# Optimization experiments

Hardware: AMD Instinct MI355X
Metric: run time of the kernel (lower is better)

Reference implementation:

```python
import jax, jax.numpy as jnp
import numpy as np

N = 8192
IN_DIM = 512
OUT_DIM = 512
TASK_DIM = 64
NEG_INF = -9.0e15  # matches torch's -9000000000000000.0 mask value


def setup_inputs() -> dict:
    key = jax.random.key(0)
    ks = jax.random.split(key, 12)
    def lin(k, fan_in, fan_out):
        kw, kb = jax.random.split(k)
        bound = 1.0 / np.sqrt(fan_in)
        W = jax.random.uniform(kw, (fan_in, fan_out), minval=-bound, maxval=bound, dtype=jnp.float32)
        b = jax.random.uniform(kb, (fan_out,), minval=-bound, maxval=bound, dtype=jnp.float32)
        return W, b
    h = jax.random.normal(ks[0], (N, IN_DIM), dtype=jnp.float32)
    z = jax.random.normal(ks[1], (N, TASK_DIM), dtype=jnp.float32)
    adj = jax.random.randint(ks[2], (N, N), 0, 2, dtype=jnp.int32)
    Wm, bm = lin(ks[3], IN_DIM, OUT_DIM)
    Wg, bg = lin(ks[4], IN_DIM + TASK_DIM, OUT_DIM)
    Wk, bk = lin(ks[5], IN_DIM, OUT_DIM)
    Wq, bq = lin(ks[6], OUT_DIM, OUT_DIM)
    a = jax.random.normal(ks[7], (OUT_DIM * 2, 1), dtype=jnp.float32)
    return {"h": h, "adj": adj, "z": z, "Wm": Wm, "bm": bm, "Wg": Wg, "bg": bg,
            "Wk": Wk, "bk": bk, "Wq": Wq, "bq": bq, "a": a}


def reference(h, adj, z, Wm, bm, Wg, bg, Wk, bk, Wq, bq, a):
    # raw message + task-conditioned gate
    raw_message = jax.nn.relu(h @ Wm + bm)                       # [N, D]
    gate = jax.nn.sigmoid(jnp.concatenate([h, z], axis=1) @ Wg + bg)  # [N, D]
    gated_message = gate * raw_message                           # [N, D]
    gate_l1_loss = jnp.sum(jnp.abs(gate)) / gate.size
    # attention scores: e[i,j] = leaky_relu(k_j . a[:D] + q_i . a[D:])
    # (decomposes the [N,N,2D] concat @ a without materializing it)
    q = gated_message @ Wq + bq                                  # [N, D]
    k = h @ Wk + bk                                              # [N, D]
    sk = k @ a[:OUT_DIM, 0]                                      # [N] key term (varies over j)
    sq = q @ a[OUT_DIM:, 0]                                      # [N] query term (varies over i)
    e = jax.nn.leaky_relu(sq[:, None] + sk[None, :])             # [N, N]
    attention = jnp.where(adj > 0, e, NEG_INF)
    attention = jax.nn.softmax(attention, axis=1)                # [N, N]
    agg_message = attention.T @ gated_message                    # [N, D]
    h_new = (agg_message + h) / 2
    return h_new, gate_l1_loss
```

## Files before the change

kernel.cpp:

```cpp
#include <hip/hip_runtime.h>

typedef unsigned short u16;
typedef unsigned char u8;
typedef unsigned long long u64;
typedef short s16x8 __attribute__((ext_vector_type(8)));
typedef float f32x4 __attribute__((ext_vector_type(4)));
typedef int i32x4 __attribute__((ext_vector_type(4)));
typedef int i32x8 __attribute__((ext_vector_type(8)));

#define NN 8192
#define DD 512
#define KCAT 576

__device__ __forceinline__ u16 f2bf(float f) {
  unsigned u = __float_as_uint(f);
  unsigned r = u + 0x7fffu + ((u >> 16) & 1u);
  return (u16)(r >> 16);
}
__device__ __forceinline__ float bf2f(u16 s) {
  return __uint_as_float(((unsigned)s) << 16);
}
__device__ __forceinline__ void gld16(const void* g, void* l) {
  __builtin_amdgcn_global_load_lds((const __attribute__((address_space(1))) void*)g,
                                   (__attribute__((address_space(3))) void*)l, 16, 0, 0);
}
__device__ __forceinline__ int pk8(float f0, float f1, float f2, float f3) {
  int p = __builtin_amdgcn_cvt_pk_fp8_f32(f0, f1, 0, 0);
  p = __builtin_amdgcn_cvt_pk_fp8_f32(f2, f3, p, 1);
  return p;
}

__global__ void k_prep(const float* __restrict__ Wk, const float* __restrict__ Wq,
                       const float* __restrict__ bk, const float* __restrict__ bq,
                       const float* __restrict__ a, const float* __restrict__ Wm,
                       const float* __restrict__ Wg, const float* __restrict__ h,
                       const float* __restrict__ z, float* __restrict__ wk_a,
                       float* __restrict__ wq_a, float* __restrict__ sc,
                       u16* __restrict__ WcT, u16* __restrict__ X) {
  const int b = blockIdx.x, t = threadIdx.x;
  if (b < 5) {
    if (b < 2) {
      int c = b * 256 + t;
      float s = 0.f;
      for (int d = 0; d < 512; d++) s += Wk[(size_t)c * 512 + d] * a[d];
      wk_a[c] = s;
    } else if (b < 4) {
      int c = (b - 2) * 256 + t;
      float s = 0.f;
      for (int d = 0; d < 512; d++) s += Wq[(size_t)c * 512 + d] * a[512 + d];
      wq_a[c] = s;
    } else {
      __shared__ float red[8];
      int lane = t & 63, w = t >> 6;
      float s1 = bk[t] * a[t] + bk[t + 256] * a[t + 256];
      float s2 = bq[t] * a[512 + t] + bq[t + 256] * a[768 + t];
      #pragma unroll
      for (int o = 32; o >= 1; o >>= 1) { s1 += __shfl_down(s1, o); s2 += __shfl_down(s2, o); }
      if (lane == 0) { red[w] = s1; red[4 + w] = s2; }
      __syncthreads();
      if (t == 0) {
        sc[0] = red[0] + red[1] + red[2] + red[3];
        sc[1] = red[4] + red[5] + red[6] + red[7];
      }
    }
  } else if (b < 293) {
    int tid = (b - 5) * 256 + t;
    int n = tid / 72, g = tid % 72;
    int lg = (g & ~7) | ((g & 7) ^ (n & 7));
    int k0 = lg * 8;
    s16x8 o;
    #pragma unroll
    for (int e = 0; e < 8; e++) {
      int k = k0 + e;
      float val;
      if (n < 512) val = (k < 512) ? Wm[(size_t)k * 512 + n] : 0.f;
      else         val = Wg[(size_t)k * 512 + (n - 512)];
      o[e] = (short)f2bf(val);
    }
    *(s16x8*)&WcT[(size_t)n * KCAT + g * 8] = o;
  } else {
    int tid = (b - 293) * 256 + t;
    int i = tid / 72, g = tid % 72;
    int lg = (g & ~7) | ((g & 7) ^ (i & 7));
    int k0 = lg * 8;
    s16x8 o;
    if (k0 < 512) {
      const f32x4* s = (const f32x4*)(h + (size_t)i * 512 + k0);
      f32x4 v0 = s[0], v1 = s[1];
      #pragma unroll
      for (int e = 0; e < 4; e++) { o[e] = (short)f2bf(v0[e]); o[e + 4] = (short)f2bf(v1[e]); }
    } else {
      const f32x4* s = (const f32x4*)(z + (size_t)i * 64 + (k0 - 512));
      f32x4 v0 = s[0], v1 = s[1];
      #pragma unroll
      for (int e = 0; e < 4; e++) { o[e] = (short)f2bf(v0[e]); o[e + 4] = (short)f2bf(v1[e]); }
    }
    *(s16x8*)&X[(size_t)i * KCAT + g * 8] = o;
  }
}

__global__ __launch_bounds__(256) void k_gemm1(const u16* __restrict__ X,
    const u16* __restrict__ W, const float* __restrict__ bm, const float* __restrict__ bg,
    u16* __restrict__ rm, u16* __restrict__ gate, float* __restrict__ l1part) {
  __shared__ __align__(16) u16 As[128 * 64];
  __shared__ __align__(16) u16 Bs[128 * 64];
  __shared__ float red[4];
  const int t = threadIdx.x, bid = blockIdx.x;
  const int i0 = (bid & 63) * 128, n0 = (bid >> 6) * 128;
  const int lane = t & 63, w = t >> 6;
  const int lr = lane & 15, lh = lane >> 4;
  const int wm = (w >> 1) * 64, wn = (w & 1) * 64;
  const f32x4 vz = {0.f, 0.f, 0.f, 0.f};
  f32x4 acc[4][4];
  #pragma unroll
  for (int a_ = 0; a_ < 4; a_++)
    #pragma unroll
    for (int b_ = 0; b_ < 4; b_++) acc[a_][b_] = vz;

  for (int step = 0; step < 9; step++) {
    const int kk = step * 64;
    __syncthreads();
    #pragma unroll
    for (int c = 0; c < 4; c++) {
      int L = c * 256 + t;
      int row = L >> 3, ch = L & 7;
      gld16(X + (size_t)(i0 + row) * KCAT + kk + ch * 8, &As[L * 8]);
      gld16(W + (size_t)(n0 + row) * KCAT + kk + ch * 8, &Bs[L * 8]);
    }
    asm volatile("s_waitcnt vmcnt(0)" ::: "memory");
    __syncthreads();
    #pragma unroll
    for (int ks = 0; ks < 2; ks++) {
      s16x8 af[4], bfv[4];
      #pragma unroll
      for (int mr = 0; mr < 4; mr++) {
        int row = wm + mr * 16 + lr;
        int ch = (ks * 4 + lh) ^ (row & 7);
        af[mr] = *(const s16x8*)&As[row * 64 + ch * 8];
      }
      #pragma unroll
      for (int nr = 0; nr < 4; nr++) {
        int nn = wn + nr * 16 + lr;
        int ch = (ks * 4 + lh) ^ (nn & 7);
        bfv[nr] = *(const s16x8*)&Bs[nn * 64 + ch * 8];
      }
      #pragma unroll
      for (int mr = 0; mr < 4; mr++)
        #pragma unroll
        for (int nr = 0; nr < 4; nr++)
          acc[mr][nr] = __builtin_amdgcn_mfma_f32_16x16x32_bf16(af[mr], bfv[nr], acc[mr][nr], 0, 0, 0);
    }
  }
  float lsum = 0.f;
  #pragma unroll
  for (int nr = 0; nr < 4; nr++) {
    int nn = n0 + wn + nr * 16 + lr;
    bool ismsg = nn < 512;
    float bias = ismsg ? bm[nn] : bg[nn - 512];
    #pragma unroll
    for (int mr = 0; mr < 4; mr++) {
      #pragma unroll
      for (int r = 0; r < 4; r++) {
        int row = i0 + wm + mr * 16 + lh * 4 + r;
        float v0 = acc[mr][nr][r] + bias;
        if (ismsg) {
          rm[(size_t)row * 512 + nn] = f2bf(fmaxf(v0, 0.f));
        } else {
          float g = 1.f / (1.f + __expf(-v0));
          gate[(size_t)row * 512 + (nn - 512)] = f2bf(g);
          lsum += g;
        }
      }
    }
  }
  #pragma unroll
  for (int o = 32; o >= 1; o >>= 1) lsum += __shfl_down(lsum, o);
  if (lane == 0) red[w] = lsum;
  __syncthreads();
  if (t == 0) l1part[bid] = red[0] + red[1] + red[2] + red[3];
}

__global__ __launch_bounds__(256) void k_rowact(const u16* __restrict__ rm,
    const u16* __restrict__ gate, const float* __restrict__ h,
    const float* __restrict__ wk_a, const float* __restrict__ wq_a,
    const float* __restrict__ sc, u16* __restrict__ gm, float* __restrict__ skv,
    float* __restrict__ sqv, float* __restrict__ uu, float* __restrict__ vv) {
  __shared__ float red[8];
  const int i = blockIdx.x, t = threadIdx.x;
  const int lane = t & 63, w = t >> 6;
  float sqp = 0.f, skp = 0.f;
  #pragma unroll
  for (int rep = 0; rep < 2; rep++) {
    int d = rep * 256 + t;
    float g = bf2f(gate[(size_t)i * 512 + d]);
    float r = bf2f(rm[(size_t)i * 512 + d]);
    float p = g * r;
    gm[(size_t)i * 512 + d] = f2bf(p);
    sqp += p * wq_a[d];
    skp += h[(size_t)i * 512 + d] * wk_a[d];
  }
  #pragma unroll
  for (int o = 32; o >= 1; o >>= 1) { sqp += __shfl_down(sqp, o); skp += __shfl_down(skp, o); }
  if (lane == 0) { red[w] = skp; red[4 + w] = sqp; }
  __syncthreads();
  if (t == 0) {
    float skt = red[0] + red[1] + red[2] + red[3] + sc[0];
    float sqt = red[4] + red[5] + red[6] + red[7] + sc[1];
    skv[i] = skt; sqv[i] = sqt;
    uu[i] = __expf(skt); vv[i] = __expf(0.01f * skt);
  }
}

__global__ __launch_bounds__(256) void k_pack(const int* __restrict__ adj, u64* __restrict__ bits) {
  __shared__ u16 nib[512];
  const int t = threadIdx.x;
  const size_t i = blockIdx.x;
  #pragma unroll
  for (int k = 0; k < 2; k++) {
    const int4* src = (const int4*)(adj + i * NN + (size_t)(t + 256 * k) * 16);
    unsigned m = 0;
    #pragma unroll
    for (int q = 0; q < 4; q++) {
      int4 v = src[q];
      m |= (v.x > 0 ? 1u : 0u) << (4 * q);
      m |= (v.y > 0 ? 2u : 0u) << (4 * q);
      m |= (v.z > 0 ? 4u : 0u) << (4 * q);
      m |= (v.w > 0 ? 8u : 0u) << (4 * q);
    }
    nib[k * 256 + t] = (u16)m;
  }
  __syncthreads();
  if (t < 128) bits[i * 128 + t] = *(const u64*)&nib[t * 4];
}

__global__ __launch_bounds__(256) void k_stats(const u64* __restrict__ bits,
    const float* __restrict__ sk, const float* __restrict__ uu, const float* __restrict__ vv,
    const float* __restrict__ sq, float* __restrict__ P, float* __restrict__ Q) {
  const int t = threadIdx.x, lane = t & 63, wv = t >> 6;
  const int i = blockIdx.x * 4 + wv;
  const float sqi = sq[i];
  const float nsq = -sqi;
  const u64* brow = bits + (size_t)i * 128;
  float zp = 0.f, zn = 0.f, m_loc = -3.0e38f;
  for (int k = 0; k < 128; k++) {
    u64 word = brow[k];
    float skj = sk[k * 64 + lane];
    float uj = uu[k * 64 + lane];
    float vj = vv[k * 64 + lane];
    m_loc = fmaxf(m_loc, skj);
    bool msk = (word >> lane) & 1ULL;
    bool pos = skj > nsq;
    zp += (msk && pos) ? uj : 0.f;
    zn += (msk && !pos) ? vj : 0.f;
  }
  #pragma unroll
  for (int o = 32; o >= 1; o >>= 1) {
    zp += __shfl_down(zp, o);
    zn += __shfl_down(zn, o);
    m_loc = fmaxf(m_loc, __shfl_down(m_loc, o));
  }
  if (lane == 0) {
    float xk = sqi + m_loc;
    float m_i = xk >= 0.f ? xk : 0.01f * xk;
    float ep = __expf(sqi - m_i), en = __expf(0.01f * sqi - m_i);
    float Z = ep * zp + en * zn;
    float inv = 1.0f / Z;
    P[i] = ep * inv;
    Q[i] = en * inv;
  }
}

__global__ __launch_bounds__(256) void k_tgm8(const u16* __restrict__ gm, u8* __restrict__ gmT8) {
  __shared__ __align__(16) u16 tile[64][72];
  const int bid = blockIdx.x;
  const int ti = bid & 127, td = bid >> 7;
  const int t = threadIdx.x;
  #pragma unroll
  for (int rep = 0; rep < 2; rep++) {
    int L = rep * 256 + t;
    int row = L >> 3, ch = L & 7;
    s16x8 val = *(const s16x8*)(gm + (size_t)(ti * 64 + row) * 512 + td * 64 + ch * 8);
    *(s16x8*)&tile[row][ch * 8] = val;
  }
  __syncthreads();
  const int dl = t >> 2, lc = t & 3;
  const int d = td * 64 + dl;
  const int chg = ti * 4 + lc;
  i32x4 o;
  #pragma unroll
  for (int q = 0; q < 4; q++) {
    int ib = lc * 16 + q * 4;
    o[q] = pk8(bf2f(tile[ib][dl]) * 16.f, bf2f(tile[ib + 1][dl]) * 16.f,
               bf2f(tile[ib + 2][dl]) * 16.f, bf2f(tile[ib + 3][dl]) * 16.f);
  }
  *(i32x4*)(gmT8 + (size_t)d * NN + (chg >> 3) * 128 + ((chg & 7) ^ (d & 7)) * 16) = o;
}

__global__ __launch_bounds__(256) void k_tgm(const u16* __restrict__ gm, u16* __restrict__ gmT) {
  __shared__ __align__(16) u16 tile[64][72];
  const int bid = blockIdx.x;
  const int ti = bid & 127, td = bid >> 7;
  const int t = threadIdx.x;
  #pragma unroll
  for (int rep = 0; rep < 2; rep++) {
    int L = rep * 256 + t;
    int row = L >> 3, ch = L & 7;
    s16x8 val = *(const s16x8*)(gm + (size_t)(ti * 64 + row) * 512 + td * 64 + ch * 8);
    *(s16x8*)&tile[row][ch * 8] = val;
  }
  __syncthreads();
  #pragma unroll
  for (int rep = 0; rep < 2; rep++) {
    int L = rep * 256 + t;
    int dr = L >> 3, ig = L & 7;
    int d = td * 64 + dr;
    s16x8 o;
    #pragma unroll
    for (int e = 0; e < 8; e++) o[e] = (short)tile[ig * 8 + e][dr];
    *(s16x8*)(gmT + (size_t)d * NN + ti * 64 + (ig ^ (d & 7)) * 8) = o;
  }
}

__global__ __launch_bounds__(256) void k_rowstats(const int* __restrict__ adj,
    const float* __restrict__ sk, const float* __restrict__ sq,
    u64* __restrict__ bits, float* __restrict__ P, float* __restrict__ Q) {
  __shared__ float sks[NN];
  __shared__ u64 bw[128];
  __shared__ float red[8];
  const int i = blockIdx.x, t = threadIdx.x;
  const int lane = t & 63, w = t >> 6;
  const int* arow = adj + (size_t)i * NN;
  float kmax = -3.0e38f;
  for (int c = 0; c < 32; c++) {
    int j = c * 256 + t;
    int av = arow[j];
    float skj = sk[j];
    sks[j] = skj;
    bool bit = av > 0;
    u64 m = __ballot(bit);
    if (lane == 0) bw[c * 4 + w] = m;
    if (bit) kmax = fmaxf(kmax, skj);
  }
  #pragma unroll
  for (int o = 32; o >= 1; o >>= 1) kmax = fmaxf(kmax, __shfl_down(kmax, o));
  if (lane == 0) red[w] = kmax;
  __syncthreads();
  float K = fmaxf(fmaxf(red[0], red[1]), fmaxf(red[2], red[3]));
  float sqi = sq[i];
  float xk = sqi + K;
  float m_i = xk >= 0.f ? xk : 0.01f * xk;
  float s = 0.f;
  for (int c = 0; c < 32; c++) {
    int j = c * 256 + t;
    u64 mw = bw[c * 4 + w];
    float xx = sqi + sks[j];
    float f = xx >= 0.f ? xx : 0.01f * xx;
    float e = __expf(f - m_i);
    if ((mw >> lane) & 1ULL) s += e;
  }
  #pragma unroll
  for (int o = 32; o >= 1; o >>= 1) s += __shfl_down(s, o);
  if (lane == 0) red[4 + w] = s;
  __syncthreads();
  if (t == 0) {
    float Z = red[4] + red[5] + red[6] + red[7];
    float inv = 1.0f / Z;
    P[i] = __expf(sqi - m_i) * inv;
    Q[i] = __expf(0.01f * sqi - m_i) * inv;
  }
  if (t < 128) bits[(size_t)i * 128 + t] = bw[t];
}

__global__ void k_bitT(const u64* __restrict__ bits, u64* __restrict__ bitT) {
  int wid = blockIdx.x * 4 + (threadIdx.x >> 6);
  int ti = wid & 127, tj = wid >> 7;
  int lane = threadIdx.x & 63;
  u64 w = bits[(size_t)(ti * 64 + lane) * 128 + tj];
  u64 out = 0;
  #pragma unroll
  for (int jj = 0; jj < 64; jj++) {
    u64 b = __ballot((int)((w >> jj) & 1ULL));
    if (jj == lane) out = b;
  }
  bitT[(size_t)(tj * 64 + lane) * 128 + ti] = out;
}

__global__ __launch_bounds__(256) void k_attgen8(const u64* __restrict__ bitT,
    const float* __restrict__ P, const float* __restrict__ Q, const float* __restrict__ sq,
    const float* __restrict__ u, const float* __restrict__ v, const float* __restrict__ sk,
    u8* __restrict__ attT8) {
  const int t = threadIdx.x, bid = blockIdx.x;
  const int jt = bid >> 1, ih = bid & 1;
  const int j0 = jt * 16;
  const int i0 = ih * 4096 + t * 16;
  f32x4 Pv[4], Qv[4], Sv[4];
  #pragma unroll
  for (int q = 0; q < 4; q++) {
    Pv[q] = *(const f32x4*)(P + i0 + q * 4);
    Qv[q] = *(const f32x4*)(Q + i0 + q * 4);
    Sv[q] = *(const f32x4*)(sq + i0 + q * 4);
  }
  const int widx = i0 >> 6;
  const int bsh = (t & 3) * 16;
  const int chg = i0 >> 4;
  const int wnd = chg >> 3, cs = chg & 7;
  #pragma unroll 2
  for (int r = 0; r < 16; r++) {
    const int j = j0 + r;
    const float uj = u[j] * 256.f, vj = v[j] * 256.f, nskj = -sk[j];
    const u64 w64 = bitT[(size_t)j * 128 + widx];
    const unsigned m16 = (unsigned)(w64 >> bsh) & 0xFFFFu;
    i32x4 o;
    #pragma unroll
    for (int q = 0; q < 4; q++) {
      float f[4];
      #pragma unroll
      for (int e = 0; e < 4; e++) {
        bool pos = Sv[q][e] > nskj;
        float val = pos ? Pv[q][e] * uj : Qv[q][e] * vj;
        f[e] = ((m16 >> (q * 4 + e)) & 1u) ? val : 0.f;
      }
      o[q] = pk8(f[0], f[1], f[2], f[3]);
    }
    *(i32x4*)(attT8 + (size_t)j * NN + wnd * 128 + ((cs ^ (j & 7)) * 16)) = o;
  }
}

__device__ __forceinline__ i32x8 ld_frag8(const u8* base, int row, int lh) {
  const int c0 = ((2 * lh) ^ (row & 7)) * 16;
  const int c1 = ((2 * lh + 1) ^ (row & 7)) * 16;
  i32x4 lo = *(const i32x4*)(base + row * 128 + c0);
  i32x4 hi = *(const i32x4*)(base + row * 128 + c1);
  i32x8 r;
  r[0] = lo[0]; r[1] = lo[1]; r[2] = lo[2]; r[3] = lo[3];
  r[4] = hi[0]; r[5] = hi[1]; r[6] = hi[2]; r[7] = hi[3];
  return r;
}

__global__ __launch_bounds__(256) void k_aggr8(const u8* __restrict__ attT8,
    const u8* __restrict__ gmT8, u16* __restrict__ pb) {
  __shared__ __align__(16) u8 As[128 * 128];
  __shared__ __align__(16) u8 Bs[128 * 128];
  const int t = threadIdx.x, bid = blockIdx.x;
  const int lid = (bid & 7) * 128 + (bid >> 3);
  const int dt = lid & 3, jt = (lid >> 2) & 63, split = lid >> 8;
  const int j0 = jt * 128, d0 = dt * 128;
  const int lane = t & 63, w = t >> 6;
  const int lr = lane & 15, lh = lane >> 4;
  const int wm = (w >> 1) * 64, wn = (w & 1) * 64;
  const f32x4 vz = {0.f, 0.f, 0.f, 0.f};
  f32x4 acc[4][4];
  #pragma unroll
  for (int a_ = 0; a_ < 4; a_++)
    #pragma unroll
    for (int b_ = 0; b_ < 4; b_++) acc[a_][b_] = vz;

  for (int step = 0; step < 16; step++) {
    const int ss = split * 16 + step;
    __syncthreads();
    #pragma unroll
    for (int c = 0; c < 4; c++) {
      int idx = c * 256 + t;
      int row = idx >> 3, ch = idx & 7;
      gld16(attT8 + (size_t)(j0 + row) * NN + (size_t)ss * 128 + ch * 16, &As[idx * 16]);
      gld16(gmT8 + (size_t)(d0 + row) * NN + (size_t)ss * 128 + ch * 16, &Bs[idx * 16]);
    }
    asm volatile("s_waitcnt vmcnt(0)" ::: "memory");
    __syncthreads();
    i32x8 af[4], bfv[4];
    #pragma unroll
    for (int mr = 0; mr < 4; mr++) af[mr] = ld_frag8(As, wm + mr * 16 + lr, lh);
    #pragma unroll
    for (int nr = 0; nr < 4; nr++) bfv[nr] = ld_frag8(Bs, wn + nr * 16 + lr, lh);
    #pragma unroll
    for (int mr = 0; mr < 4; mr++)
      #pragma unroll
      for (int nr = 0; nr < 4; nr++)
        acc[mr][nr] = __builtin_amdgcn_mfma_scale_f32_16x16x128_f8f6f4(
            af[mr], bfv[nr], acc[mr][nr], 0, 0,
            0, 0x77777777,
            0, 0x7B7B7B7B);
  }
  u16* pbs = pb + (size_t)split * NN * 512;
  #pragma unroll
  for (int mr = 0; mr < 4; mr++) {
    #pragma unroll
    for (int nr = 0; nr < 4; nr++) {
      int dn = d0 + wn + nr * 16 + lr;
      #pragma unroll
      for (int r = 0; r < 4; r++) {
        int jj = j0 + wm + mr * 16 + lh * 4 + r;
        pbs[(size_t)jj * 512 + dn] = f2bf(acc[mr][nr][r]);
      }
    }
  }
}

__global__ __launch_bounds__(512) void k_aggr(const u16* __restrict__ gmT,
    const u64* __restrict__ bitT, const float* __restrict__ P, const float* __restrict__ Q,
    const float* __restrict__ sq, const float* __restrict__ u, const float* __restrict__ v,
    const float* __restrict__ sk, u16* __restrict__ pb) {
  __shared__ __align__(16) u16 Alds[128 * 64];
  __shared__ __align__(16) u16 Blds[128 * 64];
  const int t = threadIdx.x, bid = blockIdx.x;
  const int lid = (bid & 7) * 128 + (bid >> 3);
  const int j_t = lid & 63, rest = lid >> 6;
  const int split = rest & 3, d_t = rest >> 2;
  const int j0 = j_t * 128, d0 = d_t * 128;
  const int lane = t & 63, w = t >> 6;
  const int lr = lane & 15, lh = lane >> 4;
  const int wm = (w >> 1) * 32, wn = (w & 1) * 64;
  const int gj = t & 127, gq = t >> 7;
  const int jg = j0 + gj;
  const float uj = u[jg], vj = v[jg], nskj = -sk[jg];
  const u64* btrow = bitT + (size_t)jg * 128;
  const f32x4 vzero = {0.f, 0.f, 0.f, 0.f};
  f32x4 acc[2][4];
  #pragma unroll
  for (int a_ = 0; a_ < 2; a_++)
    #pragma unroll
    for (int b_ = 0; b_ < 4; b_++) acc[a_][b_] = vzero;

  for (int step = 0; step < 32; step++) {
    const int ss = split * 32 + step;
    __syncthreads();
    #pragma unroll
    for (int c = 0; c < 2; c++) {
      int L = c * 512 + t;
      int dd = L >> 3, ch = L & 7;
      gld16(gmT + (size_t)(d0 + dd) * NN + ss * 64 + ch * 8, &Blds[L * 8]);
    }
    u64 word = btrow[ss];
    #pragma unroll
    for (int cc = 0; cc < 2; cc++) {
      int ig = gq + cc * 4;
      int i8 = ss * 64 + ig * 8;
      const f32x4* P4 = (const f32x4*)(P + i8);
      const f32x4* Q4 = (const f32x4*)(Q + i8);
      const f32x4* S4 = (const f32x4*)(sq + i8);
      s16x8 rr;
      #pragma unroll
      for (int hf = 0; hf < 2; hf++) {
        f32x4 pv = P4[hf], qv = Q4[hf], sv = S4[hf];
        #pragma unroll
        for (int e = 0; e < 4; e++) {
          int ie = hf * 4 + e;
          float val = (sv[e] > nskj) ? pv[e] * uj : qv[e] * vj;
          bool bit = (word >> (ig * 8 + ie)) & 1ULL;
          rr[ie] = bit ? (short)f2bf(val) : (short)0;
        }
      }
      *(s16x8*)&Alds[gj * 64 + (ig ^ (gj & 7)) * 8] = rr;
    }
    asm volatile("s_waitcnt vmcnt(0)" ::: "memory");
    __syncthreads();
    #pragma unroll
    for (int ks = 0; ks < 2; ks++) {
      s16x8 af[2], bfv[4];
      #pragma unroll
      for (int mr = 0; mr < 2; mr++) {
        int row = wm + mr * 16 + lr;
        int ch = (ks * 4 + lh) ^ (row & 7);
        af[mr] = *(const s16x8*)&Alds[row * 64 + ch * 8];
      }
      #pragma unroll
      for (int nr = 0; nr < 4; nr++) {
        int dn = wn + nr * 16 + lr;
        int ch = (ks * 4 + lh) ^ (dn & 7);
        bfv[nr] = *(const s16x8*)&Blds[dn * 64 + ch * 8];
      }
      #pragma unroll
      for (int mr = 0; mr < 2; mr++)
        #pragma unroll
        for (int nr = 0; nr < 4; nr++)
          acc[mr][nr] = __builtin_amdgcn_mfma_f32_16x16x32_bf16(af[mr], bfv[nr], acc[mr][nr], 0, 0, 0);
    }
  }
  u16* pbs = pb + (size_t)split * NN * 512;
  #pragma unroll
  for (int mr = 0; mr < 2; mr++) {
    #pragma unroll
    for (int nr = 0; nr < 4; nr++) {
      int dn = d0 + wn + nr * 16 + lr;
      #pragma unroll
      for (int r = 0; r < 4; r++) {
        int jj = j0 + wm + mr * 16 + lh * 4 + r;
        pbs[(size_t)jj * 512 + dn] = f2bf(acc[mr][nr][r]);
      }
    }
  }
}

__global__ __launch_bounds__(256) void k_reduce(const u16* __restrict__ pb,
    const float* __restrict__ h, float* __restrict__ out) {
  size_t base = ((size_t)blockIdx.x * 256 + threadIdx.x) * 8;
  s16x8 p0 = *(const s16x8*)(pb + base);
  s16x8 p1 = *(const s16x8*)(pb + (size_t)NN * 512 + base);
  s16x8 p2 = *(const s16x8*)(pb + (size_t)2 * NN * 512 + base);
  s16x8 p3 = *(const s16x8*)(pb + (size_t)3 * NN * 512 + base);
  f32x4 h0 = *(const f32x4*)(h + base);
  f32x4 h1 = *(const f32x4*)(h + base + 4);
  f32x4 o0, o1;
  #pragma unroll
  for (int e = 0; e < 4; e++) {
    o0[e] = (bf2f((u16)p0[e]) + bf2f((u16)p1[e]) + bf2f((u16)p2[e]) + bf2f((u16)p3[e]) + h0[e]) * 0.5f;
    o1[e] = (bf2f((u16)p0[e + 4]) + bf2f((u16)p1[e + 4]) + bf2f((u16)p2[e + 4]) + bf2f((u16)p3[e + 4]) + h1[e]) * 0.5f;
  }
  *(f32x4*)(out + base) = o0;
  *(f32x4*)(out + base + 4) = o1;
}

__global__ void k_loss(const float* __restrict__ part, float* __restrict__ out) {
  __shared__ float red[4];
  int t = threadIdx.x, lane = t & 63, w = t >> 6;
  float s = part[t] + part[t + 256];
  #pragma unroll
  for (int o = 32; o >= 1; o >>= 1) s += __shfl_down(s, o);
  if (lane == 0) red[w] = s;
  __syncthreads();
  if (t == 0) out[(size_t)NN * 512] = (red[0] + red[1] + red[2] + red[3]) * (1.0f / 4194304.0f);
}

extern "C" void kernel_launch(void* const* d_in, const int* in_sizes, int n_in,
                              void* d_out, int out_size, void* d_ws, size_t ws_size,
                              hipStream_t stream) {
  const float* h  = (const float*)d_in[0];
  const int*   adj= (const int*)d_in[1];
  const float* z  = (const float*)d_in[2];
  const float* Wm = (const float*)d_in[3];
  const float* bm = (const float*)d_in[4];
  const float* Wg = (const float*)d_in[5];
  const float* bg = (const float*)d_in[6];
  const float* Wk = (const float*)d_in[7];
  const float* bk = (const float*)d_in[8];
  const float* Wq = (const float*)d_in[9];
  const float* bq = (const float*)d_in[10];
  const float* a  = (const float*)d_in[11];
  float* out = (float*)d_out;
  char* ws = (char*)d_ws;

  size_t off = 0;
  auto alloc = [&](size_t b) { size_t o = off; off += (b + 255) & ~(size_t)255; return o; };
  float* wk_a = (float*)(ws + alloc(512 * 4));
  float* wq_a = (float*)(ws + alloc(512 * 4));
  float* sc   = (float*)(ws + alloc(256));
  float* skv  = (float*)(ws + alloc(NN * 4));
  float* sqv  = (float*)(ws + alloc(NN * 4));
  float* uu   = (float*)(ws + alloc(NN * 4));
  float* vv   = (float*)(ws + alloc(NN * 4));
  float* Pp   = (float*)(ws + alloc(NN * 4));
  float* Qp   = (float*)(ws + alloc(NN * 4));
  float* l1p  = (float*)(ws + alloc(512 * 4));
  u16*   WcT  = (u16*)(ws + alloc((size_t)1024 * KCAT * 2));
  u16*   gmTb = (u16*)(ws + alloc((size_t)DD * NN * 2));
  u64*   bitTb= (u64*)(ws + alloc((size_t)NN * 128 * 8));
  u16*   pb   = (u16*)(ws + alloc((size_t)4 * NN * 512 * 2));

  const size_t bigNeed = (size_t)NN * NN * 2;
  bool bigPath = (ws_size >= off + bigNeed);

  if (bigPath) {
    char* big = ws + alloc(bigNeed);
    u16* Xbf  = (u16*)big;
    u16* rm   = (u16*)(big + ((size_t)10 << 20));
    u16* gate = (u16*)(big + ((size_t)19 << 20));
    u16* gm   = (u16*)(big + ((size_t)28 << 20));
    u64* bits = (u64*)big;
    u8*  attT8= (u8*)big;
    u8*  gmT8 = (u8*)gmTb;

    k_prep<<<2597, 256, 0, stream>>>(Wk, Wq, bk, bq, a, Wm, Wg, h, z,
                                     wk_a, wq_a, sc, WcT, Xbf);
    k_gemm1<<<512, 256, 0, stream>>>(Xbf, WcT, bm, bg, rm, gate, l1p);
    k_rowact<<<8192, 256, 0, stream>>>(rm, gate, h, wk_a, wq_a, sc, gm, skv, sqv, uu, vv);
    k_pack<<<8192, 256, 0, stream>>>(adj, bits);
    k_stats<<<2048, 256, 0, stream>>>(bits, skv, uu, vv, sqv, Pp, Qp);
    k_tgm8<<<1024, 256, 0, stream>>>(gm, gmT8);
    k_bitT<<<4096, 256, 0, stream>>>(bits, bitTb);
    k_attgen8<<<1024, 256, 0, stream>>>(bitTb, Pp, Qp, sqv, uu, vv, skv, attT8);
    k_aggr8<<<1024, 256, 0, stream>>>(attT8, gmT8, pb);
    k_reduce<<<2048, 256, 0, stream>>>(pb, h, out);
    k_loss<<<1, 256, 0, stream>>>(l1p, out);
  } else {
    char* regA = ws + alloc((size_t)NN * KCAT * 2);
    char* regB = ws + alloc((size_t)NN * 512 * 2);
    char* regC = ws + alloc((size_t)NN * 512 * 2);
    u16* Xbf = (u16*)regA;  u64* bits = (u64*)regA;
    u16* rm  = (u16*)regB;
    u16* gate= (u16*)regC;
    u16* gmv = (u16*)(ws + alloc((size_t)NN * 512 * 2));
    k_prep<<<2597, 256, 0, stream>>>(Wk, Wq, bk, bq, a, Wm, Wg, h, z,
                                     wk_a, wq_a, sc, WcT, Xbf);
    k_gemm1<<<512, 256, 0, stream>>>(Xbf, WcT, bm, bg, rm, gate, l1p);
    k_rowact<<<8192, 256, 0, stream>>>(rm, gate, h, wk_a, wq_a, sc, gmv, skv, sqv, uu, vv);
    k_tgm<<<1024, 256, 0, stream>>>(gmv, gmTb);
    k_rowstats<<<8192, 256, 0, stream>>>(adj, skv, sqv, bits, Pp, Qp);
    k_bitT<<<4096, 256, 0, stream>>>(bits, bitTb);
    k_aggr<<<1024, 512, 0, stream>>>(gmTb, bitTb, Pp, Qp, sqv, uu, vv, skv, pb);
    k_reduce<<<2048, 256, 0, stream>>>(pb, h, out);
    k_loss<<<1, 256, 0, stream>>>(l1p, out);
  }
}
```

Baseline: 246.9 us.

## Fuse adjacency packing with row stats, merge transposes, fold loss into reduce

Computes the softmax row statistics (masked positive/negative partition sums and max key score) directly while packing the int32 adjacency into bits, so the separate stats kernel that re-read the packed bits is removed. The gm transpose-to-int8 and the bit-matrix transpose are merged into one launch split by block index, and the scalar L1 loss reduction becomes an extra block of the final reduce kernel. This cuts kernel launches and a pass over the packed bits. In exchange each packing thread now also loads sk/u/v vectors and does more ALU work per adjacency element.

```diff
diff --git a/kernel.cpp b/kernel.cpp
--- a/kernel.cpp
+++ b/kernel.cpp
@@ -211,89 +211,119 @@
   }
 }
 
-__global__ __launch_bounds__(256) void k_pack(const int* __restrict__ adj, u64* __restrict__ bits) {
+__global__ __launch_bounds__(256) void k_packstats(const int* __restrict__ adj,
+    const float* __restrict__ sk, const float* __restrict__ uu, const float* __restrict__ vv,
+    const float* __restrict__ sq, u64* __restrict__ bits,
+    float* __restrict__ P, float* __restrict__ Q) {
   __shared__ u16 nib[512];
-  const int t = threadIdx.x;
+  __shared__ float red[12];
+  const int t = threadIdx.x, lane = t & 63, w = t >> 6;
   const size_t i = blockIdx.x;
+  const float sqi = sq[i];
+  const float nsq = -sqi;
+  float zp = 0.f, zn = 0.f, mx = -3.0e38f;
   #pragma unroll
   for (int k = 0; k < 2; k++) {
-    const int4* src = (const int4*)(adj + i * NN + (size_t)(t + 256 * k) * 16);
+    const int j16 = (t + 256 * k) * 16;
+    const int4* src = (const int4*)(adj + i * NN + j16);
     unsigned m = 0;
     #pragma unroll
     for (int q = 0; q < 4; q++) {
       int4 v = src[q];
-      m |= (v.x > 0 ? 1u : 0u) << (4 * q);
-      m |= (v.y > 0 ? 2u : 0u) << (4 * q);
-      m |= (v.z > 0 ? 4u : 0u) << (4 * q);
-      m |= (v.w > 0 ? 8u : 0u) << (4 * q);
+      const int jb = j16 + q * 4;
+      f32x4 s4 = *(const f32x4*)(sk + jb);
+      f32x4 u4 = *(const f32x4*)(uu + jb);
+      f32x4 w4 = *(const f32x4*)(vv + jb);
+      int av0 = v.x, av1 = v.y, av2 = v.z, av3 = v.w;
+      bool b0 = av0 > 0, b1 = av1 > 0, b2 = av2 > 0, b3 = av3 > 0;
+      m |= (b0 ? 1u : 0u) << (q * 4);
+      m |= (b1 ? 2u : 0u) << (q * 4);
+      m |= (b2 ? 4u : 0u) << (q * 4);
+      m |= (b3 ? 8u : 0u) << (q * 4);
+      mx = fmaxf(fmaxf(mx, fmaxf(s4[0], s4[1])), fmaxf(s4[2], s4[3]));
+      bool p0 = s4[0] > nsq, p1 = s4[1] > nsq, p2 = s4[2] > nsq, p3 = s4[3] > nsq;
+      zp += (b0 && p0) ? u4[0] : 0.f;  zn += (b0 && !p0) ? w4[0] : 0.f;
+      zp += (b1 && p1) ? u4[1] : 0.f;  zn += (b1 && !p1) ? w4[1] : 0.f;
+      zp += (b2 && p2) ? u4[2] : 0.f;  zn += (b2 && !p2) ? w4[2] : 0.f;
+      zp += (b3 && p3) ? u4[3] : 0.f;  zn += (b3 && !p3) ? w4[3] : 0.f;
     }
     nib[k * 256 + t] = (u16)m;
-  }
-  __syncthreads();
-  if (t < 128) bits[i * 128 + t] = *(const u64*)&nib[t * 4];
-}
-
-__global__ __launch_bounds__(256) void k_stats(const u64* __restrict__ bits,
-    const float* __restrict__ sk, const float* __restrict__ uu, const float* __restrict__ vv,
-    const float* __restrict__ sq, float* __restrict__ P, float* __restrict__ Q) {
-  const int t = threadIdx.x, lane = t & 63, wv = t >> 6;
-  const int i = blockIdx.x * 4 + wv;
-  const float sqi = sq[i];
-  const float nsq = -sqi;
-  const u64* brow = bits + (size_t)i * 128;
-  float zp = 0.f, zn = 0.f, m_loc = -3.0e38f;
-  for (int k = 0; k < 128; k++) {
-    u64 word = brow[k];
-    float skj = sk[k * 64 + lane];
-    float uj = uu[k * 64 + lane];
-    float vj = vv[k * 64 + lane];
-    m_loc = fmaxf(m_loc, skj);
-    bool msk = (word >> lane) & 1ULL;
-    bool pos = skj > nsq;
-    zp += (msk && pos) ? uj : 0.f;
-    zn += (msk && !pos) ? vj : 0.f;
   }
   #pragma unroll
   for (int o = 32; o >= 1; o >>= 1) {
     zp += __shfl_down(zp, o);
     zn += __shfl_down(zn, o);
-    m_loc = fmaxf(m_loc, __shfl_down(m_loc, o));
-  }
-  if (lane == 0) {
-    float xk = sqi + m_loc;
+    mx = fmaxf(mx, __shfl_down(mx, o));
+  }
+  if (lane == 0) { red[w] = zp; red[4 + w] = zn; red[8 + w] = mx; }
+  __syncthreads();
+  if (t == 0) {
+    float ZP = red[0] + red[1] + red[2] + red[3];
+    float ZN = red[4] + red[5] + red[6] + red[7];
+    float MX = fmaxf(fmaxf(red[8], red[9]), fmaxf(red[10], red[11]));
+    float xk = sqi + MX;
     float m_i = xk >= 0.f ? xk : 0.01f * xk;
     float ep = __expf(sqi - m_i), en = __expf(0.01f * sqi - m_i);
-    float Z = ep * zp + en * zn;
+    float Z = ep * ZP + en * ZN;
     float inv = 1.0f / Z;
     P[i] = ep * inv;
     Q[i] = en * inv;
   }
-}
-
-__global__ __launch_bounds__(256) void k_tgm8(const u16* __restrict__ gm, u8* __restrict__ gmT8) {
-  __shared__ __align__(16) u16 tile[64][72];
-  const int bid = blockIdx.x;
-  const int ti = bid & 127, td = bid >> 7;
-  const int t = threadIdx.x;
-  #pragma unroll
-  for (int rep = 0; rep < 2; rep++) {
-    int L = rep * 256 + t;
-    int row = L >> 3, ch = L & 7;
-    s16x8 val = *(const s16x8*)(gm + (size_t)(ti * 64 + row) * 512 + td * 64 + ch * 8);
-    *(s16x8*)&tile[row][ch * 8] = val;
-  }
-  __syncthreads();
-  const int dl = t >> 2, lc = t & 3;
-  const int d = td * 64 + dl;
-  const int chg = ti * 4 + lc;
-  i32x4 o;
-  #pragma unroll
-  for (int q = 0; q < 4; q++) {
-    int ib = lc * 16 + q * 4;
-    o[q] = pk8(bf2f(tile[ib][dl]) * 16.f, bf2f(tile[ib + 1][dl]) * 16.f,
-               bf2f(tile[ib + 2][dl]) * 16.f, bf2f(tile[ib + 3][dl]) * 16.f);
-  }
-  *(i32x4*)(gmT8 + (size_t)d * NN + (chg >> 3) * 128 + ((chg & 7) ^ (d & 7)) * 16) = o;
+  if (t < 128) bits[i * 128 + t] = *(const u64*)&nib[t * 4];
+}
+
+__global__ void k_bitT(const u64* __restrict__ bits, u64* __restrict__ bitT) {
+  int wid = blockIdx.x * 4 + (threadIdx.x >> 6);
+  int ti = wid & 127, tj = wid >> 7;
+  int lane = threadIdx.x & 63;
+  u64 w = bits[(size_t)(ti * 64 + lane) * 128 + tj];
+  u64 out = 0;
+  #pragma unroll
+  for (int jj = 0; jj < 64; jj++) {
+    u64 b = __ballot((int)((w >> jj) & 1ULL));
+    if (jj == lane) out = b;
+  }
+  bitT[(size_t)(tj * 64 + lane) * 128 + ti] = out;
+}
+
+__global__ __launch_bounds__(256) void k_tb(const u16* __restrict__ gm, u8* __restrict__ gmT8,
+                                            const u64* __restrict__ bits, u64* __restrict__ bitT) {
+  const int bid = blockIdx.x, t = threadIdx.x;
+  if (bid < 1024) {
+    __shared__ __align__(16) u16 tile[64][72];
+    const int ti = bid & 127, td = bid >> 7;
+    #pragma unroll
+    for (int rep = 0; rep < 2; rep++) {
+      int L = rep * 256 + t;
+      int row = L >> 3, ch = L & 7;
+      s16x8 val = *(const s16x8*)(gm + (size_t)(ti * 64 + row) * 512 + td * 64 + ch * 8);
+      *(s16x8*)&tile[row][ch * 8] = val;
+    }
+    __syncthreads();
+    const int dl = t >> 2, lc = t & 3;
+    const int d = td * 64 + dl;
+    const int chg = ti * 4 + lc;
+    i32x4 o;
+    #pragma unroll
+    for (int q = 0; q < 4; q++) {
+      int ib = lc * 16 + q * 4;
+      o[q] = pk8(bf2f(tile[ib][dl]) * 16.f, bf2f(tile[ib + 1][dl]) * 16.f,
+                 bf2f(tile[ib + 2][dl]) * 16.f, bf2f(tile[ib + 3][dl]) * 16.f);
+    }
+    *(i32x4*)(gmT8 + (size_t)d * NN + (chg >> 3) * 128 + ((chg & 7) ^ (d & 7)) * 16) = o;
+  } else {
+    int wid = (bid - 1024) * 4 + (t >> 6);
+    int ti = wid & 127, tj = wid >> 7;
+    int lane = t & 63;
+    u64 w = bits[(size_t)(ti * 64 + lane) * 128 + tj];
+    u64 out = 0;
+    #pragma unroll
+    for (int jj = 0; jj < 64; jj++) {
+      u64 b = __ballot((int)((w >> jj) & 1ULL));
+      if (jj == lane) out = b;
+    }
+    bitT[(size_t)(tj * 64 + lane) * 128 + ti] = out;
+  }
 }
 
 __global__ __launch_bounds__(256) void k_tgm(const u16* __restrict__ gm, u16* __restrict__ gmT) {
@@ -369,20 +399,6 @@
     Q[i] = __expf(0.01f * sqi - m_i) * inv;
   }
   if (t < 128) bits[(size_t)i * 128 + t] = bw[t];
-}
-
-__global__ void k_bitT(const u64* __restrict__ bits, u64* __restrict__ bitT) {
-  int wid = blockIdx.x * 4 + (threadIdx.x >> 6);
-  int ti = wid & 127, tj = wid >> 7;
-  int lane = threadIdx.x & 63;
-  u64 w = bits[(size_t)(ti * 64 + lane) * 128 + tj];
-  u64 out = 0;
-  #pragma unroll
-  for (int jj = 0; jj < 64; jj++) {
-    u64 b = __ballot((int)((w >> jj) & 1ULL));
-    if (jj == lane) out = b;
-  }
-  bitT[(size_t)(tj * 64 + lane) * 128 + ti] = out;
 }
 
 __global__ __launch_bounds__(256) void k_attgen8(const u64* __restrict__ bitT,
@@ -592,7 +608,18 @@
 }
 
 __global__ __launch_bounds__(256) void k_reduce(const u16* __restrict__ pb,
-    const float* __restrict__ h, float* __restrict__ out) {
+    const float* __restrict__ h, const float* __restrict__ part, float* __restrict__ out) {
+  if (blockIdx.x == 2048) {
+    __shared__ float red[4];
+    int t = threadIdx.x, lane = t & 63, w = t >> 6;
+    float s = part[t] + part[t + 256];
+    #pragma unroll
+    for (int o = 32; o >= 1; o >>= 1) s += __shfl_down(s, o);
+    if (lane == 0) red[w] = s;
+    __syncthreads();
+    if (t == 0) out[(size_t)NN * 512] = (red[0] + red[1] + red[2] + red[3]) * (1.0f / 4194304.0f);
+    return;
+  }
   size_t base = ((size_t)blockIdx.x * 256 + threadIdx.x) * 8;
   s16x8 p0 = *(const s16x8*)(pb + base);
   s16x8 p1 = *(const s16x8*)(pb + (size_t)NN * 512 + base);
@@ -608,17 +635,6 @@
   }
   *(f32x4*)(out + base) = o0;
   *(f32x4*)(out + base + 4) = o1;
-}
-
-__global__ void k_loss(const float* __restrict__ part, float* __restrict__ out) {
-  __shared__ float red[4];
-  int t = threadIdx.x, lane = t & 63, w = t >> 6;
-  float s = part[t] + part[t + 256];
-  #pragma unroll
-  for (int o = 32; o >= 1; o >>= 1) s += __shfl_down(s, o);
-  if (lane == 0) red[w] = s;
-  __syncthreads();
-  if (t == 0) out[(size_t)NN * 512] = (red[0] + red[1] + red[2] + red[3]) * (1.0f / 4194304.0f);
 }
 
 extern "C" void kernel_launch(void* const* d_in, const int* in_sizes, int n_in,
@@ -673,14 +689,11 @@
                                      wk_a, wq_a, sc, WcT, Xbf);
     k_gemm1<<<512, 256, 0, stream>>>(Xbf, WcT, bm, bg, rm, gate, l1p);
     k_rowact<<<8192, 256, 0, stream>>>(rm, gate, h, wk_a, wq_a, sc, gm, skv, sqv, uu, vv);
-    k_pack<<<8192, 256, 0, stream>>>(adj, bits);
-    k_stats<<<2048, 256, 0, stream>>>(bits, skv, uu, vv, sqv, Pp, Qp);
-    k_tgm8<<<1024, 256, 0, stream>>>(gm, gmT8);
-    k_bitT<<<4096, 256, 0, stream>>>(bits, bitTb);
+    k_packstats<<<8192, 256, 0, stream>>>(adj, skv, uu, vv, sqv, bits, Pp, Qp);
+    k_tb<<<5120, 256, 0, stream>>>(gm, gmT8, bits, bitTb);
     k_attgen8<<<1024, 256, 0, stream>>>(bitTb, Pp, Qp, sqv, uu, vv, skv, attT8);
     k_aggr8<<<1024, 256, 0, stream>>>(attT8, gmT8, pb);
-    k_reduce<<<2048, 256, 0, stream>>>(pb, h, out);
-    k_loss<<<1, 256, 0, stream>>>(l1p, out);
+    k_reduce<<<2049, 256, 0, stream>>>(pb, h, l1p, out);
   } else {
     char* regA = ws + alloc((size_t)NN * KCAT * 2);
     char* regB = ws + alloc((size_t)NN * 512 * 2);
@@ -697,7 +710,6 @@
     k_rowstats<<<8192, 256, 0, stream>>>(adj, skv, sqv, bits, Pp, Qp);
     k_bitT<<<4096, 256, 0, stream>>>(bits, bitTb);
     k_aggr<<<1024, 512, 0, stream>>>(gmTb, bitTb, Pp, Qp, sqv, uu, vv, skv, pb);
-    k_reduce<<<2048, 256, 0, stream>>>(pb, h, out);
-    k_loss<<<1, 256, 0, stream>>>(l1p, out);
-  }
-}
+    k_reduce<<<2049, 256, 0, stream>>>(pb, h, l1p, out);
+  }
+}
```

Result: slower. 272.6 us (+10.4%).
